# Kernel tuning notes

Hardware: AMD Instinct MI355X
Metric: run time of the kernel (lower is better)

Reference implementation:

```python
import jax, jax.numpy as jnp
import numpy as np

NEG_INF = -1e6  # d2l masked_softmax mask value

def setup_inputs() -> dict:
    key = jax.random.key(0)
    ks = jax.random.split(key, 6)
    B, Lq, Lk, dq, dv, H = 8, 256, 512, 256, 256, 64
    return {
        "queries": jax.random.normal(ks[0], (B, Lq, dq), jnp.float32),
        "keys": jax.random.normal(ks[1], (B, Lk, dq), jnp.float32),
        "values": jax.random.normal(ks[2], (B, Lk, dv), jnp.float32),
        "valid_lens": jax.random.randint(ks[3], (B,), 0, Lk),
        "W_q": jax.random.normal(ks[4], (H, dq), jnp.float32) * (dq ** -0.5),
        "W_k": jax.random.normal(ks[5], (H, dq), jnp.float32) * (dq ** -0.5),
        "w_v": jax.random.normal(jax.random.fold_in(key, 7), (H,), jnp.float32) * (H ** -0.5),
    }

def reference(queries, keys, values, valid_lens, W_q, W_k, w_v):
    # Project: [B,Lq,H], [B,Lk,H]
    q = jnp.einsum('bqd,hd->bqh', queries, W_q)
    k = jnp.einsum('bkd,hd->bkh', keys, W_k)
    # Broadcast-add + tanh: [B,Lq,Lk,H]
    features = jnp.tanh(q[:, :, None, :] + k[:, None, :, :])
    # Scalar projection -> scores [B,Lq,Lk]
    scores = jnp.einsum('bqkh,h->bqk', features, w_v)
    # masked_softmax over last axis with per-batch valid_lens
    Lk = keys.shape[1]
    mask = jnp.arange(Lk)[None, None, :] < valid_lens[:, None, None]
    scores = jnp.where(mask, scores, NEG_INF)
    attn = jax.nn.softmax(scores, axis=-1)
    # dropout p=0 (inference) -> identity; bmm with values
    return jnp.einsum('bqk,bkv->bqv', attn, values)
```

## Files before the change

### kernel.cpp

```cpp
#include <hip/hip_runtime.h>
#include <hip/hip_bf16.h>
#include <hip/hip_fp16.h>
#include <stdint.h>

#define NB 8
#define LQ 256
#define LK 512
#define NH 64
#define SCALE 2.8853900817779268f
#define L2E 1.4426950408889634f

#define QP_OFF   0
#define KP_OFF   131072
#define VBF_OFF  393216
#define PL_OFF   917504

extern "C" __device__ float __ocml_exp2_f32(float);
static __device__ __forceinline__ float fexp2(float x) {
#if __has_builtin(__builtin_amdgcn_exp2f)
  return __builtin_amdgcn_exp2f(x);
#else
  return __ocml_exp2_f32(x);
#endif
}
static __device__ __forceinline__ float frcp(float x) {
  return __builtin_amdgcn_rcpf(x);
}
static __device__ __forceinline__ uint16_t f2bf(float f) {
  uint32_t u = __float_as_uint(f);
  uint32_t r = (u + 0x7FFFu + ((u >> 16) & 1u)) >> 16;
  return (uint16_t)r;
}

typedef const __attribute__((address_space(1))) void* gas_ptr;
typedef __attribute__((address_space(3))) void* las_ptr;
static __device__ __forceinline__ void gload16(const void* g, void* l) {
  __builtin_amdgcn_global_load_lds((gas_ptr)g, (las_ptr)l, 16, 0, 0);
}

__global__ __launch_bounds__(256) void proj_kernel(
    const float* __restrict__ queries, const float* __restrict__ keys,
    const float* __restrict__ values,
    const float* __restrict__ Wq, const float* __restrict__ Wk,
    float* __restrict__ qp, float* __restrict__ kp, uint16_t* __restrict__ vbf)
{
  __shared__ float Wt[256][36];
  const int blk = blockIdx.x;
  const int t = threadIdx.x;

  if (blk >= 192) {
    int base = (blk - 192) * 16384 + t * 4;
#pragma unroll
    for (int it = 0; it < 16; ++it) {
      int idx = base + it * 1024;
      float4 v = *(const float4*)(values + idx);
      uint32_t lo = (uint32_t)f2bf(v.x) | ((uint32_t)f2bf(v.y) << 16);
      uint32_t hi = (uint32_t)f2bf(v.z) | ((uint32_t)f2bf(v.w) << 16);
      uint2 pk = {lo, hi};
      *(uint2*)(vbf + idx) = pk;
    }
    return;
  }

  const bool isQ = (blk < 64);
  const int sub = isQ ? blk : (blk - 64);
  const int tile = sub >> 1;
  const int hh = (sub & 1) * 32;
  const int rowbase = tile * 64;
  const float* __restrict__ X = isQ ? queries : keys;
  const float* __restrict__ W = isQ ? Wq : Wk;
  float* __restrict__ P = isQ ? qp : kp;

#pragma unroll 4
  for (int it = 0; it < 32; ++it) {
    Wt[t][it] = W[(hh + it) * 256 + t];
  }
  __syncthreads();

  const int ty = t >> 3;
  const int tx = t & 7;
  float a0x = 0.f, a0y = 0.f, a0z = 0.f, a0w = 0.f;
  float a1x = 0.f, a1y = 0.f, a1z = 0.f, a1w = 0.f;

  const float* xr0 = X + (size_t)(rowbase + ty * 2) * 256;
  const float* xr1 = xr0 + 256;

#pragma unroll 4
  for (int d4 = 0; d4 < 64; ++d4) {
    int d = d4 * 4;
    float4 x0 = *(const float4*)(xr0 + d);
    float4 x1 = *(const float4*)(xr1 + d);
    float4 w0 = *(const float4*)&Wt[d + 0][tx * 4];
    float4 w1 = *(const float4*)&Wt[d + 1][tx * 4];
    float4 w2 = *(const float4*)&Wt[d + 2][tx * 4];
    float4 w3 = *(const float4*)&Wt[d + 3][tx * 4];
#define STEP(XC, WD) \
    a0x = fmaf(x0.XC, WD.x, a0x); a0y = fmaf(x0.XC, WD.y, a0y); \
    a0z = fmaf(x0.XC, WD.z, a0z); a0w = fmaf(x0.XC, WD.w, a0w); \
    a1x = fmaf(x1.XC, WD.x, a1x); a1y = fmaf(x1.XC, WD.y, a1y); \
    a1z = fmaf(x1.XC, WD.z, a1z); a1w = fmaf(x1.XC, WD.w, a1w);
    STEP(x, w0) STEP(y, w1) STEP(z, w2) STEP(w, w3)
#undef STEP
  }

  {
    int row0 = rowbase + ty * 2;
    int h = hh + tx * 4;
    float4 o0 = {a0x * SCALE, a0y * SCALE, a0z * SCALE, a0w * SCALE};
    float4 o1 = {a1x * SCALE, a1y * SCALE, a1z * SCALE, a1w * SCALE};
    *(float4*)&P[(size_t)row0 * 64 + h] = o0;
    *(float4*)&P[(size_t)(row0 + 1) * 64 + h] = o1;
  }
}

__global__ __launch_bounds__(256) void attn_kernel(
    const float* __restrict__ qp, const float* __restrict__ kp,
    const uint16_t* __restrict__ vbf, const float* __restrict__ w_v,
    const int* __restrict__ valid_lens, float* __restrict__ out,
    float* __restrict__ pl, float* __restrict__ pacc, int nsplit)
{
  __shared__ float kTs[2][32][64];
  __shared__ uint16_t Vs[2][32][256];
  __shared__ float p_s[4][2][32];

  const int t = threadIdx.x;
  const int lane = t & 63;
  const int w = t >> 6;
  const int r2 = lane >> 5;
  const int kx = lane & 31;
  const int wg = blockIdx.x;
  const int b = wg & 7;
  const int qg = (wg >> 3) & 31;
  const int kh = wg >> 8;
  const int row = b * LQ + qg * 8 + w * 2 + r2;

  const int vl = valid_lens[b];
  const int n = (vl > 0) ? vl : LK;
  const int span = LK / nsplit;
  const int kstart = kh * span;
  int cnt = n - kstart;
  if (cnt > span) cnt = span;
  const int ntiles = (cnt > 0) ? ((cnt + 31) >> 5) : 0;

  if (ntiles == 0) {
    if (kx == 0) pl[row * nsplit + kh] = 0.f;
    float4 z = {0.f, 0.f, 0.f, 0.f};
    float* pa = pacc + ((size_t)(row * nsplit + kh)) * 256 + kx * 8;
    *(float4*)(pa + 0) = z;
    *(float4*)(pa + 4) = z;
    return;
  }

  float W1 = 0.f;
#pragma unroll
  for (int g = 0; g < 16; ++g) {
    float4 wf = *(const float4*)(w_v + g * 4);
    W1 += (wf.x + wf.y) + (wf.z + wf.w);
  }
  const float W1L = W1 * L2E;

  float qv[64];
  {
    const float* qrow = qp + (size_t)row * 64;
#pragma unroll
    for (int i = 0; i < 16; ++i) {
      float4 v = *(const float4*)(qrow + i * 4);
      qv[i * 4 + 0] = v.x; qv[i * 4 + 1] = v.y;
      qv[i * 4 + 2] = v.z; qv[i * 4 + 3] = v.w;
    }
  }

  const float* kpb = kp + (size_t)(b * LK) * 64;
  const char* vbc = (const char*)(vbf + (size_t)b * LK * 256);

#define STAGE(BUF, K0) do { \
    int i0 = w * 2; \
    int kjr0 = i0 * 4 + (lane >> 4); \
    int cph = lane & 15; \
    gload16(kpb + (size_t)((K0) + kjr0) * 64 + (cph ^ (kjr0 & 7)) * 4, \
            &kTs[BUF][i0 * 4][0]); \
    int kjr1 = kjr0 + 4; \
    gload16(kpb + (size_t)((K0) + kjr1) * 64 + (cph ^ (kjr1 & 7)) * 4, \
            &kTs[BUF][i0 * 4 + 4][0]); \
    const char* vsrc = vbc + (size_t)(K0) * 512 + (size_t)w * 4096 + lane * 16; \
    gload16(vsrc + 0 * 1024, &Vs[BUF][w * 8 + 0][0]); \
    gload16(vsrc + 1 * 1024, &Vs[BUF][w * 8 + 2][0]); \
    gload16(vsrc + 2 * 1024, &Vs[BUF][w * 8 + 4][0]); \
    gload16(vsrc + 3 * 1024, &Vs[BUF][w * 8 + 6][0]); \
  } while (0)

  float l = 0.f;
  float acc[16];
#pragma unroll
  for (int i = 0; i < 16; ++i) acc[i] = 0.f;

  STAGE(0, kstart);

  for (int tt = 0; tt < ntiles; ++tt) {
    const int cur = tt & 1;
    const int k0 = kstart + tt * 32;
    if (tt + 1 < ntiles) {
      STAGE(cur ^ 1, k0 + 32);
      asm volatile("s_waitcnt vmcnt(6)" ::: "memory");
    } else {
      asm volatile("s_waitcnt vmcnt(0)" ::: "memory");
    }
    __builtin_amdgcn_sched_barrier(0);
    __builtin_amdgcn_s_barrier();
    __builtin_amdgcn_sched_barrier(0);
    __builtin_amdgcn_s_setprio(1);

    float r0 = 0.f, r1 = 0.f, r2a = 0.f, r3 = 0.f;
#pragma unroll
    for (int g = 0; g < 16; ++g) {
      float4 kf = *(const float4*)&kTs[cur][kx][((g ^ (kx & 7)) << 2)];
      float4 wf = *(const float4*)(w_v + g * 4);
      r0  = fmaf(wf.x, frcp(1.f + fexp2(qv[g * 4 + 0] + kf.x)), r0);
      r1  = fmaf(wf.y, frcp(1.f + fexp2(qv[g * 4 + 1] + kf.y)), r1);
      r2a = fmaf(wf.z, frcp(1.f + fexp2(qv[g * 4 + 2] + kf.z)), r2a);
      r3  = fmaf(wf.w, frcp(1.f + fexp2(qv[g * 4 + 3] + kf.w)), r3);
    }
    float racc = (r0 + r1) + (r2a + r3);

    float pe = fexp2(fmaf(-SCALE, racc, W1L));
    int kg = k0 + kx;
    float p;
    if (vl == 0)      p = 1.f;
    else if (kg < n)  p = pe;
    else              p = 0.f;

    l += p;
    p_s[w][r2][kx] = p;

    const int c = kx;
#pragma unroll
    for (int i4 = 0; i4 < 4; ++i4) {
      float4 p0 = *(const float4*)&p_s[w][0][r2 * 16 + i4 * 4];
      float4 p1 = *(const float4*)&p_s[w][1][r2 * 16 + i4 * 4];
#pragma unroll
      for (int jj = 0; jj < 4; ++jj) {
        int kk = r2 * 16 + i4 * 4 + jj;
        uint4 vv = *(const uint4*)&Vs[cur][kk][c * 8];
        float pj0 = (jj == 0) ? p0.x : (jj == 1) ? p0.y : (jj == 2) ? p0.z : p0.w;
        float pj1 = (jj == 0) ? p1.x : (jj == 1) ? p1.y : (jj == 2) ? p1.z : p1.w;
        float f0 = __uint_as_float(vv.x << 16);
        float f1 = __uint_as_float(vv.x & 0xFFFF0000u);
        float f2 = __uint_as_float(vv.y << 16);
        float f3 = __uint_as_float(vv.y & 0xFFFF0000u);
        float f4 = __uint_as_float(vv.z << 16);
        float f5 = __uint_as_float(vv.z & 0xFFFF0000u);
        float f6 = __uint_as_float(vv.w << 16);
        float f7 = __uint_as_float(vv.w & 0xFFFF0000u);
        acc[0] = fmaf(pj0, f0, acc[0]);   acc[8]  = fmaf(pj1, f0, acc[8]);
        acc[1] = fmaf(pj0, f1, acc[1]);   acc[9]  = fmaf(pj1, f1, acc[9]);
        acc[2] = fmaf(pj0, f2, acc[2]);   acc[10] = fmaf(pj1, f2, acc[10]);
        acc[3] = fmaf(pj0, f3, acc[3]);   acc[11] = fmaf(pj1, f3, acc[11]);
        acc[4] = fmaf(pj0, f4, acc[4]);   acc[12] = fmaf(pj1, f4, acc[12]);
        acc[5] = fmaf(pj0, f5, acc[5]);   acc[13] = fmaf(pj1, f5, acc[13]);
        acc[6] = fmaf(pj0, f6, acc[6]);   acc[14] = fmaf(pj1, f6, acc[14]);
        acc[7] = fmaf(pj0, f7, acc[7]);   acc[15] = fmaf(pj1, f7, acc[15]);
      }
    }
    __builtin_amdgcn_s_setprio(0);
    __builtin_amdgcn_sched_barrier(0);
    __builtin_amdgcn_s_barrier();
  }
#undef STAGE

#pragma unroll
  for (int i = 0; i < 16; ++i) acc[i] += __shfl_xor(acc[i], 32, 64);
#pragma unroll
  for (int s = 16; s; s >>= 1) l += __shfl_xor(l, s, 64);

  const float* accr = acc + r2 * 8;
  if (nsplit == 1) {
    float inv = 1.f / l;
    float4 o0 = {accr[0] * inv, accr[1] * inv, accr[2] * inv, accr[3] * inv};
    float4 o1 = {accr[4] * inv, accr[5] * inv, accr[6] * inv, accr[7] * inv};
    float* op = out + (size_t)row * 256 + kx * 8;
    *(float4*)(op + 0) = o0;
    *(float4*)(op + 4) = o1;
  } else {
    if (kx == 0) pl[row * nsplit + kh] = l;
    float* pa = pacc + ((size_t)(row * nsplit + kh)) * 256 + kx * 8;
    float4 a0 = {accr[0], accr[1], accr[2], accr[3]};
    float4 a1 = {accr[4], accr[5], accr[6], accr[7]};
    *(float4*)(pa + 0) = a0;
    *(float4*)(pa + 4) = a1;
  }
}

__global__ __launch_bounds__(256) void merge_kernel(
    const float* __restrict__ pl, const float* __restrict__ pacc,
    float* __restrict__ out, int nsplit)
{
  const int t = threadIdx.x;
  const int row = blockIdx.x * 8 + (t >> 5);
  const int d8 = t & 31;

  float L = 0.f;
  float o[8];
#pragma unroll
  for (int i = 0; i < 8; ++i) o[i] = 0.f;

  for (int kh = 0; kh < nsplit; ++kh) {
    L += pl[row * nsplit + kh];
    const float* pa = pacc + ((size_t)(row * nsplit + kh)) * 256 + d8 * 8;
    float4 a0 = *(const float4*)(pa + 0);
    float4 a1 = *(const float4*)(pa + 4);
    o[0] += a0.x; o[1] += a0.y; o[2] += a0.z; o[3] += a0.w;
    o[4] += a1.x; o[5] += a1.y; o[6] += a1.z; o[7] += a1.w;
  }
  float inv = 1.f / L;
  float4 o0 = {o[0] * inv, o[1] * inv, o[2] * inv, o[3] * inv};
  float4 o1 = {o[4] * inv, o[5] * inv, o[6] * inv, o[7] * inv};
  float* op = out + (size_t)row * 256 + d8 * 8;
  *(float4*)(op + 0) = o0;
  *(float4*)(op + 4) = o1;
}

extern "C" void kernel_launch(void* const* d_in, const int* in_sizes, int n_in,
                              void* d_out, int out_size, void* d_ws, size_t ws_size,
                              hipStream_t stream) {
  const float* queries    = (const float*)d_in[0];
  const float* keys       = (const float*)d_in[1];
  const float* values     = (const float*)d_in[2];
  const int*   valid_lens = (const int*)d_in[3];
  const float* Wq         = (const float*)d_in[4];
  const float* Wk         = (const float*)d_in[5];
  const float* w_v        = (const float*)d_in[6];
  float* out = (float*)d_out;

  float* ws = (float*)d_ws;
  float* qp  = ws + QP_OFF;
  float* kp  = ws + KP_OFF;
  uint16_t* vbf = (uint16_t*)(ws + VBF_OFF);
  float* pl  = ws + PL_OFF;

  int nsplit;
  if      (ws_size >= (size_t)PL_OFF * 4 + 2048u * 4 * 4 + 2048u * 4 * 1024) nsplit = 4;
  else if (ws_size >= (size_t)PL_OFF * 4 + 2048u * 2 * 4 + 2048u * 2 * 1024) nsplit = 2;
  else nsplit = 1;
  float* pacc = pl + (size_t)2048 * nsplit;

  hipLaunchKernelGGL(proj_kernel, dim3(256), dim3(256), 0, stream,
                     queries, keys, values, Wq, Wk, qp, kp, vbf);
  hipLaunchKernelGGL(attn_kernel, dim3(nsplit * 256), dim3(256), 0, stream,
                     qp, kp, vbf, w_v, valid_lens, out, pl, pacc, nsplit);
  if (nsplit > 1) {
    hipLaunchKernelGGL(merge_kernel, dim3(256), dim3(256), 0, stream,
                       pl, pacc, out, nsplit);
  }
}
```

Baseline: 43.37 us.

## Use persistent attention blocks with an atomic work counter for load balancing

Replaces the one-block-per-unit grid with a fixed grid of 768 persistent blocks that pull (batch, query-group, key-split) work units from a global atomic counter reset by a memset before launch. The aim is to balance uneven per-unit work caused by variable valid_lens, and to let blocks that finish early on masked-out units pick up more work. It costs an extra memset launch, an atomic plus two block barriers per unit, and possibly worse register or scheduling behaviour from wrapping the kernel body in a loop.

New measurement: 44.92 us. +3.6%, slower.

```diff
diff --git a/kernel.cpp b/kernel.cpp
--- a/kernel.cpp
+++ b/kernel.cpp
@@ -13,7 +13,7 @@
 #define QP_OFF   0
 #define KP_OFF   131072
 #define VBF_OFF  393216
-#define PL_OFF   917504
+#define CTR_OFF  917504
 
 extern "C" __device__ float __ocml_exp2_f32(float);
 static __device__ __forceinline__ float fexp2(float x) {
@@ -117,39 +117,21 @@
     const float* __restrict__ qp, const float* __restrict__ kp,
     const uint16_t* __restrict__ vbf, const float* __restrict__ w_v,
     const int* __restrict__ valid_lens, float* __restrict__ out,
-    float* __restrict__ pl, float* __restrict__ pacc, int nsplit)
+    uint32_t* __restrict__ ctr, float* __restrict__ pl,
+    float* __restrict__ pacc, int nsplit)
 {
   __shared__ float kTs[2][32][64];
   __shared__ uint16_t Vs[2][32][256];
   __shared__ float p_s[4][2][32];
+  __shared__ uint32_t unit_s;
 
   const int t = threadIdx.x;
   const int lane = t & 63;
   const int w = t >> 6;
   const int r2 = lane >> 5;
   const int kx = lane & 31;
-  const int wg = blockIdx.x;
-  const int b = wg & 7;
-  const int qg = (wg >> 3) & 31;
-  const int kh = wg >> 8;
-  const int row = b * LQ + qg * 8 + w * 2 + r2;
-
-  const int vl = valid_lens[b];
-  const int n = (vl > 0) ? vl : LK;
+  const uint32_t NU = 256u * (uint32_t)nsplit;
   const int span = LK / nsplit;
-  const int kstart = kh * span;
-  int cnt = n - kstart;
-  if (cnt > span) cnt = span;
-  const int ntiles = (cnt > 0) ? ((cnt + 31) >> 5) : 0;
-
-  if (ntiles == 0) {
-    if (kx == 0) pl[row * nsplit + kh] = 0.f;
-    float4 z = {0.f, 0.f, 0.f, 0.f};
-    float* pa = pacc + ((size_t)(row * nsplit + kh)) * 256 + kx * 8;
-    *(float4*)(pa + 0) = z;
-    *(float4*)(pa + 4) = z;
-    return;
-  }
 
   float W1 = 0.f;
 #pragma unroll
@@ -159,19 +141,47 @@
   }
   const float W1L = W1 * L2E;
 
-  float qv[64];
-  {
-    const float* qrow = qp + (size_t)row * 64;
-#pragma unroll
-    for (int i = 0; i < 16; ++i) {
-      float4 v = *(const float4*)(qrow + i * 4);
-      qv[i * 4 + 0] = v.x; qv[i * 4 + 1] = v.y;
-      qv[i * 4 + 2] = v.z; qv[i * 4 + 3] = v.w;
-    }
-  }
-
-  const float* kpb = kp + (size_t)(b * LK) * 64;
-  const char* vbc = (const char*)(vbf + (size_t)b * LK * 256);
+  for (;;) {
+    if (t == 0) unit_s = atomicAdd(ctr, 1u);
+    __syncthreads();
+    const uint32_t u = unit_s;
+    __syncthreads();
+    if (u >= NU) break;
+
+    const int b = u & 7;
+    const int qg = (u >> 3) & 31;
+    const int kh = u >> 8;
+    const int row = b * LQ + qg * 8 + w * 2 + r2;
+
+    const int vl = valid_lens[b];
+    const int n = (vl > 0) ? vl : LK;
+    const int kstart = kh * span;
+    int cnt = n - kstart;
+    if (cnt > span) cnt = span;
+    const int ntiles = (cnt > 0) ? ((cnt + 31) >> 5) : 0;
+
+    if (ntiles == 0) {
+      if (kx == 0) pl[row * nsplit + kh] = 0.f;
+      float4 z = {0.f, 0.f, 0.f, 0.f};
+      float* pa = pacc + ((size_t)(row * nsplit + kh)) * 256 + kx * 8;
+      *(float4*)(pa + 0) = z;
+      *(float4*)(pa + 4) = z;
+      continue;
+    }
+
+    float qv[64];
+    {
+      const float* qrow = qp + (size_t)row * 64;
+#pragma unroll
+      for (int i = 0; i < 16; ++i) {
+        float4 v = *(const float4*)(qrow + i * 4);
+        qv[i * 4 + 0] = v.x; qv[i * 4 + 1] = v.y;
+        qv[i * 4 + 2] = v.z; qv[i * 4 + 3] = v.w;
+      }
+    }
+
+    const float* kpb = kp + (size_t)(b * LK) * 64;
+    const char* vbc = (const char*)(vbf + (size_t)b * LK * 256);
 
 #define STAGE(BUF, K0) do { \
     int i0 = w * 2; \
@@ -189,104 +199,105 @@
     gload16(vsrc + 3 * 1024, &Vs[BUF][w * 8 + 6][0]); \
   } while (0)
 
-  float l = 0.f;
-  float acc[16];
-#pragma unroll
-  for (int i = 0; i < 16; ++i) acc[i] = 0.f;
-
-  STAGE(0, kstart);
-
-  for (int tt = 0; tt < ntiles; ++tt) {
-    const int cur = tt & 1;
-    const int k0 = kstart + tt * 32;
-    if (tt + 1 < ntiles) {
-      STAGE(cur ^ 1, k0 + 32);
-      asm volatile("s_waitcnt vmcnt(6)" ::: "memory");
+    float l = 0.f;
+    float acc[16];
+#pragma unroll
+    for (int i = 0; i < 16; ++i) acc[i] = 0.f;
+
+    STAGE(0, kstart);
+
+    for (int tt = 0; tt < ntiles; ++tt) {
+      const int cur = tt & 1;
+      const int k0 = kstart + tt * 32;
+      if (tt + 1 < ntiles) {
+        STAGE(cur ^ 1, k0 + 32);
+        asm volatile("s_waitcnt vmcnt(6)" ::: "memory");
+      } else {
+        asm volatile("s_waitcnt vmcnt(0)" ::: "memory");
+      }
+      __builtin_amdgcn_sched_barrier(0);
+      __builtin_amdgcn_s_barrier();
+      __builtin_amdgcn_sched_barrier(0);
+      __builtin_amdgcn_s_setprio(1);
+
+      float r0 = 0.f, r1 = 0.f, r2a = 0.f, r3 = 0.f;
+#pragma unroll
+      for (int g = 0; g < 16; ++g) {
+        float4 kf = *(const float4*)&kTs[cur][kx][((g ^ (kx & 7)) << 2)];
+        float4 wf = *(const float4*)(w_v + g * 4);
+        r0  = fmaf(wf.x, frcp(1.f + fexp2(qv[g * 4 + 0] + kf.x)), r0);
+        r1  = fmaf(wf.y, frcp(1.f + fexp2(qv[g * 4 + 1] + kf.y)), r1);
+        r2a = fmaf(wf.z, frcp(1.f + fexp2(qv[g * 4 + 2] + kf.z)), r2a);
+        r3  = fmaf(wf.w, frcp(1.f + fexp2(qv[g * 4 + 3] + kf.w)), r3);
+      }
+      float racc = (r0 + r1) + (r2a + r3);
+
+      float pe = fexp2(fmaf(-SCALE, racc, W1L));
+      int kg = k0 + kx;
+      float p;
+      if (vl == 0)      p = 1.f;
+      else if (kg < n)  p = pe;
+      else              p = 0.f;
+
+      l += p;
+      p_s[w][r2][kx] = p;
+
+      const int c = kx;
+#pragma unroll
+      for (int i4 = 0; i4 < 4; ++i4) {
+        float4 p0 = *(const float4*)&p_s[w][0][r2 * 16 + i4 * 4];
+        float4 p1 = *(const float4*)&p_s[w][1][r2 * 16 + i4 * 4];
+#pragma unroll
+        for (int jj = 0; jj < 4; ++jj) {
+          int kk = r2 * 16 + i4 * 4 + jj;
+          uint4 vv = *(const uint4*)&Vs[cur][kk][c * 8];
+          float pj0 = (jj == 0) ? p0.x : (jj == 1) ? p0.y : (jj == 2) ? p0.z : p0.w;
+          float pj1 = (jj == 0) ? p1.x : (jj == 1) ? p1.y : (jj == 2) ? p1.z : p1.w;
+          float f0 = __uint_as_float(vv.x << 16);
+          float f1 = __uint_as_float(vv.x & 0xFFFF0000u);
+          float f2 = __uint_as_float(vv.y << 16);
+          float f3 = __uint_as_float(vv.y & 0xFFFF0000u);
+          float f4 = __uint_as_float(vv.z << 16);
+          float f5 = __uint_as_float(vv.z & 0xFFFF0000u);
+          float f6 = __uint_as_float(vv.w << 16);
+          float f7 = __uint_as_float(vv.w & 0xFFFF0000u);
+          acc[0] = fmaf(pj0, f0, acc[0]);   acc[8]  = fmaf(pj1, f0, acc[8]);
+          acc[1] = fmaf(pj0, f1, acc[1]);   acc[9]  = fmaf(pj1, f1, acc[9]);
+          acc[2] = fmaf(pj0, f2, acc[2]);   acc[10] = fmaf(pj1, f2, acc[10]);
+          acc[3] = fmaf(pj0, f3, acc[3]);   acc[11] = fmaf(pj1, f3, acc[11]);
+          acc[4] = fmaf(pj0, f4, acc[4]);   acc[12] = fmaf(pj1, f4, acc[12]);
+          acc[5] = fmaf(pj0, f5, acc[5]);   acc[13] = fmaf(pj1, f5, acc[13]);
+          acc[6] = fmaf(pj0, f6, acc[6]);   acc[14] = fmaf(pj1, f6, acc[14]);
+          acc[7] = fmaf(pj0, f7, acc[7]);   acc[15] = fmaf(pj1, f7, acc[15]);
+        }
+      }
+      __builtin_amdgcn_s_setprio(0);
+      __builtin_amdgcn_sched_barrier(0);
+      __builtin_amdgcn_s_barrier();
+    }
+#undef STAGE
+
+#pragma unroll
+    for (int i = 0; i < 16; ++i) acc[i] += __shfl_xor(acc[i], 32, 64);
+#pragma unroll
+    for (int s = 16; s; s >>= 1) l += __shfl_xor(l, s, 64);
+
+    const float* accr = acc + r2 * 8;
+    if (nsplit == 1) {
+      float inv = 1.f / l;
+      float4 o0 = {accr[0] * inv, accr[1] * inv, accr[2] * inv, accr[3] * inv};
+      float4 o1 = {accr[4] * inv, accr[5] * inv, accr[6] * inv, accr[7] * inv};
+      float* op = out + (size_t)row * 256 + kx * 8;
+      *(float4*)(op + 0) = o0;
+      *(float4*)(op + 4) = o1;
     } else {
-      asm volatile("s_waitcnt vmcnt(0)" ::: "memory");
-    }
-    __builtin_amdgcn_sched_barrier(0);
-    __builtin_amdgcn_s_barrier();
-    __builtin_amdgcn_sched_barrier(0);
-    __builtin_amdgcn_s_setprio(1);
-
-    float r0 = 0.f, r1 = 0.f, r2a = 0.f, r3 = 0.f;
-#pragma unroll
-    for (int g = 0; g < 16; ++g) {
-      float4 kf = *(const float4*)&kTs[cur][kx][((g ^ (kx & 7)) << 2)];
-      float4 wf = *(const float4*)(w_v + g * 4);
-      r0  = fmaf(wf.x, frcp(1.f + fexp2(qv[g * 4 + 0] + kf.x)), r0);
-      r1  = fmaf(wf.y, frcp(1.f + fexp2(qv[g * 4 + 1] + kf.y)), r1);
-      r2a = fmaf(wf.z, frcp(1.f + fexp2(qv[g * 4 + 2] + kf.z)), r2a);
-      r3  = fmaf(wf.w, frcp(1.f + fexp2(qv[g * 4 + 3] + kf.w)), r3);
-    }
-    float racc = (r0 + r1) + (r2a + r3);
-
-    float pe = fexp2(fmaf(-SCALE, racc, W1L));
-    int kg = k0 + kx;
-    float p;
-    if (vl == 0)      p = 1.f;
-    else if (kg < n)  p = pe;
-    else              p = 0.f;
-
-    l += p;
-    p_s[w][r2][kx] = p;
-
-    const int c = kx;
-#pragma unroll
-    for (int i4 = 0; i4 < 4; ++i4) {
-      float4 p0 = *(const float4*)&p_s[w][0][r2 * 16 + i4 * 4];
-      float4 p1 = *(const float4*)&p_s[w][1][r2 * 16 + i4 * 4];
-#pragma unroll
-      for (int jj = 0; jj < 4; ++jj) {
-        int kk = r2 * 16 + i4 * 4 + jj;
-        uint4 vv = *(const uint4*)&Vs[cur][kk][c * 8];
-        float pj0 = (jj == 0) ? p0.x : (jj == 1) ? p0.y : (jj == 2) ? p0.z : p0.w;
-        float pj1 = (jj == 0) ? p1.x : (jj == 1) ? p1.y : (jj == 2) ? p1.z : p1.w;
-        float f0 = __uint_as_float(vv.x << 16);
-        float f1 = __uint_as_float(vv.x & 0xFFFF0000u);
-        float f2 = __uint_as_float(vv.y << 16);
-        float f3 = __uint_as_float(vv.y & 0xFFFF0000u);
-        float f4 = __uint_as_float(vv.z << 16);
-        float f5 = __uint_as_float(vv.z & 0xFFFF0000u);
-        float f6 = __uint_as_float(vv.w << 16);
-        float f7 = __uint_as_float(vv.w & 0xFFFF0000u);
-        acc[0] = fmaf(pj0, f0, acc[0]);   acc[8]  = fmaf(pj1, f0, acc[8]);
-        acc[1] = fmaf(pj0, f1, acc[1]);   acc[9]  = fmaf(pj1, f1, acc[9]);
-        acc[2] = fmaf(pj0, f2, acc[2]);   acc[10] = fmaf(pj1, f2, acc[10]);
-        acc[3] = fmaf(pj0, f3, acc[3]);   acc[11] = fmaf(pj1, f3, acc[11]);
-        acc[4] = fmaf(pj0, f4, acc[4]);   acc[12] = fmaf(pj1, f4, acc[12]);
-        acc[5] = fmaf(pj0, f5, acc[5]);   acc[13] = fmaf(pj1, f5, acc[13]);
-        acc[6] = fmaf(pj0, f6, acc[6]);   acc[14] = fmaf(pj1, f6, acc[14]);
-        acc[7] = fmaf(pj0, f7, acc[7]);   acc[15] = fmaf(pj1, f7, acc[15]);
-      }
-    }
-    __builtin_amdgcn_s_setprio(0);
-    __builtin_amdgcn_sched_barrier(0);
-    __builtin_amdgcn_s_barrier();
-  }
-#undef STAGE
-
-#pragma unroll
-  for (int i = 0; i < 16; ++i) acc[i] += __shfl_xor(acc[i], 32, 64);
-#pragma unroll
-  for (int s = 16; s; s >>= 1) l += __shfl_xor(l, s, 64);
-
-  const float* accr = acc + r2 * 8;
-  if (nsplit == 1) {
-    float inv = 1.f / l;
-    float4 o0 = {accr[0] * inv, accr[1] * inv, accr[2] * inv, accr[3] * inv};
-    float4 o1 = {accr[4] * inv, accr[5] * inv, accr[6] * inv, accr[7] * inv};
-    float* op = out + (size_t)row * 256 + kx * 8;
-    *(float4*)(op + 0) = o0;
-    *(float4*)(op + 4) = o1;
-  } else {
-    if (kx == 0) pl[row * nsplit + kh] = l;
-    float* pa = pacc + ((size_t)(row * nsplit + kh)) * 256 + kx * 8;
-    float4 a0 = {accr[0], accr[1], accr[2], accr[3]};
-    float4 a1 = {accr[4], accr[5], accr[6], accr[7]};
-    *(float4*)(pa + 0) = a0;
-    *(float4*)(pa + 4) = a1;
+      if (kx == 0) pl[row * nsplit + kh] = l;
+      float* pa = pacc + ((size_t)(row * nsplit + kh)) * 256 + kx * 8;
+      float4 a0 = {accr[0], accr[1], accr[2], accr[3]};
+      float4 a1 = {accr[4], accr[5], accr[6], accr[7]};
+      *(float4*)(pa + 0) = a0;
+      *(float4*)(pa + 4) = a1;
+    }
   }
 }
 
@@ -335,18 +346,20 @@
   float* qp  = ws + QP_OFF;
   float* kp  = ws + KP_OFF;
   uint16_t* vbf = (uint16_t*)(ws + VBF_OFF);
-  float* pl  = ws + PL_OFF;
+  uint32_t* ctr = (uint32_t*)(ws + CTR_OFF);
 
   int nsplit;
-  if      (ws_size >= (size_t)PL_OFF * 4 + 2048u * 4 * 4 + 2048u * 4 * 1024) nsplit = 4;
-  else if (ws_size >= (size_t)PL_OFF * 4 + 2048u * 2 * 4 + 2048u * 2 * 1024) nsplit = 2;
+  if      (ws_size >= (size_t)CTR_OFF * 4 + 64 + 2048u * 4 * 4 + 2048u * 4 * 1024) nsplit = 4;
+  else if (ws_size >= (size_t)CTR_OFF * 4 + 64 + 2048u * 2 * 4 + 2048u * 2 * 1024) nsplit = 2;
   else nsplit = 1;
+  float* pl   = ws + CTR_OFF + 16;
   float* pacc = pl + (size_t)2048 * nsplit;
 
   hipLaunchKernelGGL(proj_kernel, dim3(256), dim3(256), 0, stream,
                      queries, keys, values, Wq, Wk, qp, kp, vbf);
-  hipLaunchKernelGGL(attn_kernel, dim3(nsplit * 256), dim3(256), 0, stream,
-                     qp, kp, vbf, w_v, valid_lens, out, pl, pacc, nsplit);
+  hipMemsetAsync(ctr, 0, 4, stream);
+  hipLaunchKernelGGL(attn_kernel, dim3(768), dim3(256), 0, stream,
+                     qp, kp, vbf, w_v, valid_lens, out, ctr, pl, pacc, nsplit);
   if (nsplit > 1) {
     hipLaunchKernelGGL(merge_kernel, dim3(256), dim3(256), 0, stream,
                        pl, pacc, out, nsplit);
```

## Fuse split-K merge into attention kernel via last-block atomic counter

Applied to the files above, without the earlier changes.

Removes the separate merge kernel launch. Each attention workgroup writes its partial sums, fences, and atomically increments a per-(batch, query-group) counter. The last arriving split does the reduction and normalisation. Empty splits now skip writing zero partial accumulators, and the merge skips partials whose l is zero. The counters are reset in proj_kernel, at the cost of a threadfence and atomic per block and a serialized tail merge.

Result: slower. 165.1 us (+280.7%).

```diff
diff --git a/kernel.cpp b/kernel.cpp
--- a/kernel.cpp
+++ b/kernel.cpp
@@ -42,11 +42,14 @@
     const float* __restrict__ queries, const float* __restrict__ keys,
     const float* __restrict__ values,
     const float* __restrict__ Wq, const float* __restrict__ Wk,
-    float* __restrict__ qp, float* __restrict__ kp, uint16_t* __restrict__ vbf)
+    float* __restrict__ qp, float* __restrict__ kp, uint16_t* __restrict__ vbf,
+    uint32_t* __restrict__ cnt)
 {
   __shared__ float Wt[256][36];
   const int blk = blockIdx.x;
   const int t = threadIdx.x;
+
+  if (t == 0) cnt[blk] = 0;
 
   if (blk >= 192) {
     int base = (blk - 192) * 16384 + t * 4;
@@ -117,11 +120,13 @@
     const float* __restrict__ qp, const float* __restrict__ kp,
     const uint16_t* __restrict__ vbf, const float* __restrict__ w_v,
     const int* __restrict__ valid_lens, float* __restrict__ out,
-    float* __restrict__ pl, float* __restrict__ pacc, int nsplit)
+    float* __restrict__ pl, float* __restrict__ pacc,
+    uint32_t* __restrict__ cnt, int nsplit)
 {
   __shared__ float kTs[2][32][64];
   __shared__ uint16_t Vs[2][32][256];
   __shared__ float p_s[4][2][32];
+  __shared__ uint32_t old_s;
 
   const int t = threadIdx.x;
   const int lane = t & 63;
@@ -138,40 +143,37 @@
   const int n = (vl > 0) ? vl : LK;
   const int span = LK / nsplit;
   const int kstart = kh * span;
-  int cnt = n - kstart;
-  if (cnt > span) cnt = span;
-  const int ntiles = (cnt > 0) ? ((cnt + 31) >> 5) : 0;
-
-  if (ntiles == 0) {
-    if (kx == 0) pl[row * nsplit + kh] = 0.f;
-    float4 z = {0.f, 0.f, 0.f, 0.f};
-    float* pa = pacc + ((size_t)(row * nsplit + kh)) * 256 + kx * 8;
-    *(float4*)(pa + 0) = z;
-    *(float4*)(pa + 4) = z;
-    return;
-  }
-
-  float W1 = 0.f;
-#pragma unroll
-  for (int g = 0; g < 16; ++g) {
-    float4 wf = *(const float4*)(w_v + g * 4);
-    W1 += (wf.x + wf.y) + (wf.z + wf.w);
-  }
-  const float W1L = W1 * L2E;
-
-  float qv[64];
-  {
-    const float* qrow = qp + (size_t)row * 64;
-#pragma unroll
-    for (int i = 0; i < 16; ++i) {
-      float4 v = *(const float4*)(qrow + i * 4);
-      qv[i * 4 + 0] = v.x; qv[i * 4 + 1] = v.y;
-      qv[i * 4 + 2] = v.z; qv[i * 4 + 3] = v.w;
-    }
-  }
-
-  const float* kpb = kp + (size_t)(b * LK) * 64;
-  const char* vbc = (const char*)(vbf + (size_t)b * LK * 256);
+  int cnt_k = n - kstart;
+  if (cnt_k > span) cnt_k = span;
+  const int ntiles = (cnt_k > 0) ? ((cnt_k + 31) >> 5) : 0;
+
+  float l = 0.f;
+  float acc[16];
+#pragma unroll
+  for (int i = 0; i < 16; ++i) acc[i] = 0.f;
+
+  if (ntiles > 0) {
+    float W1 = 0.f;
+#pragma unroll
+    for (int g = 0; g < 16; ++g) {
+      float4 wf = *(const float4*)(w_v + g * 4);
+      W1 += (wf.x + wf.y) + (wf.z + wf.w);
+    }
+    const float W1L = W1 * L2E;
+
+    float qv[64];
+    {
+      const float* qrow = qp + (size_t)row * 64;
+#pragma unroll
+      for (int i = 0; i < 16; ++i) {
+        float4 v = *(const float4*)(qrow + i * 4);
+        qv[i * 4 + 0] = v.x; qv[i * 4 + 1] = v.y;
+        qv[i * 4 + 2] = v.z; qv[i * 4 + 3] = v.w;
+      }
+    }
+
+    const float* kpb = kp + (size_t)(b * LK) * 64;
+    const char* vbc = (const char*)(vbf + (size_t)b * LK * 256);
 
 #define STAGE(BUF, K0) do { \
     int i0 = w * 2; \
@@ -189,88 +191,84 @@
     gload16(vsrc + 3 * 1024, &Vs[BUF][w * 8 + 6][0]); \
   } while (0)
 
-  float l = 0.f;
-  float acc[16];
-#pragma unroll
-  for (int i = 0; i < 16; ++i) acc[i] = 0.f;
-
-  STAGE(0, kstart);
-
-  for (int tt = 0; tt < ntiles; ++tt) {
-    const int cur = tt & 1;
-    const int k0 = kstart + tt * 32;
-    if (tt + 1 < ntiles) {
-      STAGE(cur ^ 1, k0 + 32);
-      asm volatile("s_waitcnt vmcnt(6)" ::: "memory");
-    } else {
-      asm volatile("s_waitcnt vmcnt(0)" ::: "memory");
-    }
-    __builtin_amdgcn_sched_barrier(0);
-    __builtin_amdgcn_s_barrier();
-    __builtin_amdgcn_sched_barrier(0);
-    __builtin_amdgcn_s_setprio(1);
-
-    float r0 = 0.f, r1 = 0.f, r2a = 0.f, r3 = 0.f;
-#pragma unroll
-    for (int g = 0; g < 16; ++g) {
-      float4 kf = *(const float4*)&kTs[cur][kx][((g ^ (kx & 7)) << 2)];
-      float4 wf = *(const float4*)(w_v + g * 4);
-      r0  = fmaf(wf.x, frcp(1.f + fexp2(qv[g * 4 + 0] + kf.x)), r0);
-      r1  = fmaf(wf.y, frcp(1.f + fexp2(qv[g * 4 + 1] + kf.y)), r1);
-      r2a = fmaf(wf.z, frcp(1.f + fexp2(qv[g * 4 + 2] + kf.z)), r2a);
-      r3  = fmaf(wf.w, frcp(1.f + fexp2(qv[g * 4 + 3] + kf.w)), r3);
-    }
-    float racc = (r0 + r1) + (r2a + r3);
-
-    float pe = fexp2(fmaf(-SCALE, racc, W1L));
-    int kg = k0 + kx;
-    float p;
-    if (vl == 0)      p = 1.f;
-    else if (kg < n)  p = pe;
-    else              p = 0.f;
-
-    l += p;
-    p_s[w][r2][kx] = p;
-
-    const int c = kx;
-#pragma unroll
-    for (int i4 = 0; i4 < 4; ++i4) {
-      float4 p0 = *(const float4*)&p_s[w][0][r2 * 16 + i4 * 4];
-      float4 p1 = *(const float4*)&p_s[w][1][r2 * 16 + i4 * 4];
-#pragma unroll
-      for (int jj = 0; jj < 4; ++jj) {
-        int kk = r2 * 16 + i4 * 4 + jj;
-        uint4 vv = *(const uint4*)&Vs[cur][kk][c * 8];
-        float pj0 = (jj == 0) ? p0.x : (jj == 1) ? p0.y : (jj == 2) ? p0.z : p0.w;
-        float pj1 = (jj == 0) ? p1.x : (jj == 1) ? p1.y : (jj == 2) ? p1.z : p1.w;
-        float f0 = __uint_as_float(vv.x << 16);
-        float f1 = __uint_as_float(vv.x & 0xFFFF0000u);
-        float f2 = __uint_as_float(vv.y << 16);
-        float f3 = __uint_as_float(vv.y & 0xFFFF0000u);
-        float f4 = __uint_as_float(vv.z << 16);
-        float f5 = __uint_as_float(vv.z & 0xFFFF0000u);
-        float f6 = __uint_as_float(vv.w << 16);
-        float f7 = __uint_as_float(vv.w & 0xFFFF0000u);
-        acc[0] = fmaf(pj0, f0, acc[0]);   acc[8]  = fmaf(pj1, f0, acc[8]);
-        acc[1] = fmaf(pj0, f1, acc[1]);   acc[9]  = fmaf(pj1, f1, acc[9]);
-        acc[2] = fmaf(pj0, f2, acc[2]);   acc[10] = fmaf(pj1, f2, acc[10]);
-        acc[3] = fmaf(pj0, f3, acc[3]);   acc[11] = fmaf(pj1, f3, acc[11]);
-        acc[4] = fmaf(pj0, f4, acc[4]);   acc[12] = fmaf(pj1, f4, acc[12]);
-        acc[5] = fmaf(pj0, f5, acc[5]);   acc[13] = fmaf(pj1, f5, acc[13]);
-        acc[6] = fmaf(pj0, f6, acc[6]);   acc[14] = fmaf(pj1, f6, acc[14]);
-        acc[7] = fmaf(pj0, f7, acc[7]);   acc[15] = fmaf(pj1, f7, acc[15]);
-      }
-    }
-    __builtin_amdgcn_s_setprio(0);
-    __builtin_amdgcn_sched_barrier(0);
-    __builtin_amdgcn_s_barrier();
-  }
+    STAGE(0, kstart);
+
+    for (int tt = 0; tt < ntiles; ++tt) {
+      const int cur = tt & 1;
+      const int k0 = kstart + tt * 32;
+      if (tt + 1 < ntiles) {
+        STAGE(cur ^ 1, k0 + 32);
+        asm volatile("s_waitcnt vmcnt(6)" ::: "memory");
+      } else {
+        asm volatile("s_waitcnt vmcnt(0)" ::: "memory");
+      }
+      __builtin_amdgcn_sched_barrier(0);
+      __builtin_amdgcn_s_barrier();
+      __builtin_amdgcn_sched_barrier(0);
+      __builtin_amdgcn_s_setprio(1);
+
+      float r0 = 0.f, r1 = 0.f, r2a = 0.f, r3 = 0.f;
+#pragma unroll
+      for (int g = 0; g < 16; ++g) {
+        float4 kf = *(const float4*)&kTs[cur][kx][((g ^ (kx & 7)) << 2)];
+        float4 wf = *(const float4*)(w_v + g * 4);
+        r0  = fmaf(wf.x, frcp(1.f + fexp2(qv[g * 4 + 0] + kf.x)), r0);
+        r1  = fmaf(wf.y, frcp(1.f + fexp2(qv[g * 4 + 1] + kf.y)), r1);
+        r2a = fmaf(wf.z, frcp(1.f + fexp2(qv[g * 4 + 2] + kf.z)), r2a);
+        r3  = fmaf(wf.w, frcp(1.f + fexp2(qv[g * 4 + 3] + kf.w)), r3);
+      }
+      float racc = (r0 + r1) + (r2a + r3);
+
+      float pe = fexp2(fmaf(-SCALE, racc, W1L));
+      int kg = k0 + kx;
+      float p;
+      if (vl == 0)      p = 1.f;
+      else if (kg < n)  p = pe;
+      else              p = 0.f;
+
+      l += p;
+      p_s[w][r2][kx] = p;
+
+      const int c = kx;
+#pragma unroll
+      for (int i4 = 0; i4 < 4; ++i4) {
+        float4 p0 = *(const float4*)&p_s[w][0][r2 * 16 + i4 * 4];
+        float4 p1 = *(const float4*)&p_s[w][1][r2 * 16 + i4 * 4];
+#pragma unroll
+        for (int jj = 0; jj < 4; ++jj) {
+          int kk = r2 * 16 + i4 * 4 + jj;
+          uint4 vv = *(const uint4*)&Vs[cur][kk][c * 8];
+          float pj0 = (jj == 0) ? p0.x : (jj == 1) ? p0.y : (jj == 2) ? p0.z : p0.w;
+          float pj1 = (jj == 0) ? p1.x : (jj == 1) ? p1.y : (jj == 2) ? p1.z : p1.w;
+          float f0 = __uint_as_float(vv.x << 16);
+          float f1 = __uint_as_float(vv.x & 0xFFFF0000u);
+          float f2 = __uint_as_float(vv.y << 16);
+          float f3 = __uint_as_float(vv.y & 0xFFFF0000u);
+          float f4 = __uint_as_float(vv.z << 16);
+          float f5 = __uint_as_float(vv.z & 0xFFFF0000u);
+          float f6 = __uint_as_float(vv.w << 16);
+          float f7 = __uint_as_float(vv.w & 0xFFFF0000u);
+          acc[0] = fmaf(pj0, f0, acc[0]);   acc[8]  = fmaf(pj1, f0, acc[8]);
+          acc[1] = fmaf(pj0, f1, acc[1]);   acc[9]  = fmaf(pj1, f1, acc[9]);
+          acc[2] = fmaf(pj0, f2, acc[2]);   acc[10] = fmaf(pj1, f2, acc[10]);
+          acc[3] = fmaf(pj0, f3, acc[3]);   acc[11] = fmaf(pj1, f3, acc[11]);
+          acc[4] = fmaf(pj0, f4, acc[4]);   acc[12] = fmaf(pj1, f4, acc[12]);
+          acc[5] = fmaf(pj0, f5, acc[5]);   acc[13] = fmaf(pj1, f5, acc[13]);
+          acc[6] = fmaf(pj0, f6, acc[6]);   acc[14] = fmaf(pj1, f6, acc[14]);
+          acc[7] = fmaf(pj0, f7, acc[7]);   acc[15] = fmaf(pj1, f7, acc[15]);
+        }
+      }
+      __builtin_amdgcn_s_setprio(0);
+      __builtin_amdgcn_sched_barrier(0);
+      __builtin_amdgcn_s_barrier();
+    }
 #undef STAGE
 
 #pragma unroll
-  for (int i = 0; i < 16; ++i) acc[i] += __shfl_xor(acc[i], 32, 64);
-#pragma unroll
-  for (int s = 16; s; s >>= 1) l += __shfl_xor(l, s, 64);
+    for (int i = 0; i < 16; ++i) acc[i] += __shfl_xor(acc[i], 32, 64);
+#pragma unroll
+    for (int s = 16; s; s >>= 1) l += __shfl_xor(l, s, 64);
+  }
 
   const float* accr = acc + r2 * 8;
   if (nsplit == 1) {
@@ -280,43 +278,50 @@
     float* op = out + (size_t)row * 256 + kx * 8;
     *(float4*)(op + 0) = o0;
     *(float4*)(op + 4) = o1;
-  } else {
-    if (kx == 0) pl[row * nsplit + kh] = l;
+    return;
+  }
+
+  if (kx == 0) pl[row * nsplit + kh] = l;
+  if (ntiles > 0) {
     float* pa = pacc + ((size_t)(row * nsplit + kh)) * 256 + kx * 8;
     float4 a0 = {accr[0], accr[1], accr[2], accr[3]};
     float4 a1 = {accr[4], accr[5], accr[6], accr[7]};
     *(float4*)(pa + 0) = a0;
     *(float4*)(pa + 4) = a1;
   }
-}
-
-__global__ __launch_bounds__(256) void merge_kernel(
-    const float* __restrict__ pl, const float* __restrict__ pacc,
-    float* __restrict__ out, int nsplit)
-{
-  const int t = threadIdx.x;
-  const int row = blockIdx.x * 8 + (t >> 5);
-  const int d8 = t & 31;
-
-  float L = 0.f;
-  float o[8];
-#pragma unroll
-  for (int i = 0; i < 8; ++i) o[i] = 0.f;
-
-  for (int kh = 0; kh < nsplit; ++kh) {
-    L += pl[row * nsplit + kh];
-    const float* pa = pacc + ((size_t)(row * nsplit + kh)) * 256 + d8 * 8;
-    float4 a0 = *(const float4*)(pa + 0);
-    float4 a1 = *(const float4*)(pa + 4);
-    o[0] += a0.x; o[1] += a0.y; o[2] += a0.z; o[3] += a0.w;
-    o[4] += a1.x; o[5] += a1.y; o[6] += a1.z; o[7] += a1.w;
-  }
-  float inv = 1.f / L;
-  float4 o0 = {o[0] * inv, o[1] * inv, o[2] * inv, o[3] * inv};
-  float4 o1 = {o[4] * inv, o[5] * inv, o[6] * inv, o[7] * inv};
-  float* op = out + (size_t)row * 256 + d8 * 8;
-  *(float4*)(op + 0) = o0;
-  *(float4*)(op + 4) = o1;
+
+  __threadfence();
+  __syncthreads();
+  if (t == 0) old_s = atomicAdd(&cnt[(b << 5) | qg], 1u);
+  __syncthreads();
+  if (old_s != (uint32_t)(nsplit - 1)) return;
+
+  __threadfence();
+  {
+    const int mrow = b * LQ + qg * 8 + (t >> 5);
+    const int d8 = t & 31;
+    float L = 0.f;
+    float o[8];
+#pragma unroll
+    for (int i = 0; i < 8; ++i) o[i] = 0.f;
+    for (int kh2 = 0; kh2 < nsplit; ++kh2) {
+      float lk = pl[mrow * nsplit + kh2];
+      if (lk > 0.f) {
+        L += lk;
+        const float* pa = pacc + ((size_t)(mrow * nsplit + kh2)) * 256 + d8 * 8;
+        float4 a0 = *(const float4*)(pa + 0);
+        float4 a1 = *(const float4*)(pa + 4);
+        o[0] += a0.x; o[1] += a0.y; o[2] += a0.z; o[3] += a0.w;
+        o[4] += a1.x; o[5] += a1.y; o[6] += a1.z; o[7] += a1.w;
+      }
+    }
+    float inv = 1.f / L;
+    float4 o0 = {o[0] * inv, o[1] * inv, o[2] * inv, o[3] * inv};
+    float4 o1 = {o[4] * inv, o[5] * inv, o[6] * inv, o[7] * inv};
+    float* op = out + (size_t)mrow * 256 + d8 * 8;
+    *(float4*)(op + 0) = o0;
+    *(float4*)(op + 4) = o1;
+  }
 }
 
 extern "C" void kernel_launch(void* const* d_in, const int* in_sizes, int n_in,
@@ -338,17 +343,14 @@
   float* pl  = ws + PL_OFF;
 
   int nsplit;
-  if      (ws_size >= (size_t)PL_OFF * 4 + 2048u * 4 * 4 + 2048u * 4 * 1024) nsplit = 4;
-  else if (ws_size >= (size_t)PL_OFF * 4 + 2048u * 2 * 4 + 2048u * 2 * 1024) nsplit = 2;
+  if      (ws_size >= (size_t)PL_OFF * 4 + 2048u * 4 * 4 + 2048u * 4 * 1024 + 1024) nsplit = 4;
+  else if (ws_size >= (size_t)PL_OFF * 4 + 2048u * 2 * 4 + 2048u * 2 * 1024 + 1024) nsplit = 2;
   else nsplit = 1;
   float* pacc = pl + (size_t)2048 * nsplit;
+  uint32_t* cnt = (uint32_t*)(pacc + (size_t)2048 * nsplit * 256);
 
   hipLaunchKernelGGL(proj_kernel, dim3(256), dim3(256), 0, stream,
-                     queries, keys, values, Wq, Wk, qp, kp, vbf);
+                     queries, keys, values, Wq, Wk, qp, kp, vbf, cnt);
   hipLaunchKernelGGL(attn_kernel, dim3(nsplit * 256), dim3(256), 0, stream,
-                     qp, kp, vbf, w_v, valid_lens, out, pl, pacc, nsplit);
-  if (nsplit > 1) {
-    hipLaunchKernelGGL(merge_kernel, dim3(256), dim3(256), 0, stream,
-                       pl, pacc, out, nsplit);
-  }
-}
+                     qp, kp, vbf, w_v, valid_lens, out, pl, pacc, cnt, nsplit);
+}
```

## Single-buffer K/V shared tiles and issue first stage before Q load

Applied to the files above, without the earlier changes.

Replaces the double-buffered K/V shared-memory staging with a single buffer. The next tile's loads are now issued only after the end-of-iteration barrier, and the loop waits for all loads before computing. The first stage is moved ahead of the W1 and Q register loads so it overlaps them. This halves LDS use, which may raise occupancy, but it gives up overlapping the next tile's global loads with the current tile's compute.

Measured after the change: 44.34 us. 2.2% more time.

```diff
diff --git a/kernel.cpp b/kernel.cpp
--- a/kernel.cpp
+++ b/kernel.cpp
@@ -119,8 +119,8 @@
     const int* __restrict__ valid_lens, float* __restrict__ out,
     float* __restrict__ pl, float* __restrict__ pacc, int nsplit)
 {
-  __shared__ float kTs[2][32][64];
-  __shared__ uint16_t Vs[2][32][256];
+  __shared__ float kTs[32][64];
+  __shared__ uint16_t Vs[32][256];
   __shared__ float p_s[4][2][32];
 
   const int t = threadIdx.x;
@@ -151,6 +151,27 @@
     return;
   }
 
+  const float* kpb = kp + (size_t)(b * LK) * 64;
+  const char* vbc = (const char*)(vbf + (size_t)b * LK * 256);
+
+#define STAGE(K0) do { \
+    int i0 = w * 2; \
+    int kjr0 = i0 * 4 + (lane >> 4); \
+    int cph = lane & 15; \
+    gload16(kpb + (size_t)((K0) + kjr0) * 64 + (cph ^ (kjr0 & 7)) * 4, \
+            &kTs[i0 * 4][0]); \
+    int kjr1 = kjr0 + 4; \
+    gload16(kpb + (size_t)((K0) + kjr1) * 64 + (cph ^ (kjr1 & 7)) * 4, \
+            &kTs[i0 * 4 + 4][0]); \
+    const char* vsrc = vbc + (size_t)(K0) * 512 + (size_t)w * 4096 + lane * 16; \
+    gload16(vsrc + 0 * 1024, &Vs[w * 8 + 0][0]); \
+    gload16(vsrc + 1 * 1024, &Vs[w * 8 + 2][0]); \
+    gload16(vsrc + 2 * 1024, &Vs[w * 8 + 4][0]); \
+    gload16(vsrc + 3 * 1024, &Vs[w * 8 + 6][0]); \
+  } while (0)
+
+  STAGE(kstart);
+
   float W1 = 0.f;
 #pragma unroll
   for (int g = 0; g < 16; ++g) {
@@ -170,41 +191,14 @@
     }
   }
 
-  const float* kpb = kp + (size_t)(b * LK) * 64;
-  const char* vbc = (const char*)(vbf + (size_t)b * LK * 256);
-
-#define STAGE(BUF, K0) do { \
-    int i0 = w * 2; \
-    int kjr0 = i0 * 4 + (lane >> 4); \
-    int cph = lane & 15; \
-    gload16(kpb + (size_t)((K0) + kjr0) * 64 + (cph ^ (kjr0 & 7)) * 4, \
-            &kTs[BUF][i0 * 4][0]); \
-    int kjr1 = kjr0 + 4; \
-    gload16(kpb + (size_t)((K0) + kjr1) * 64 + (cph ^ (kjr1 & 7)) * 4, \
-            &kTs[BUF][i0 * 4 + 4][0]); \
-    const char* vsrc = vbc + (size_t)(K0) * 512 + (size_t)w * 4096 + lane * 16; \
-    gload16(vsrc + 0 * 1024, &Vs[BUF][w * 8 + 0][0]); \
-    gload16(vsrc + 1 * 1024, &Vs[BUF][w * 8 + 2][0]); \
-    gload16(vsrc + 2 * 1024, &Vs[BUF][w * 8 + 4][0]); \
-    gload16(vsrc + 3 * 1024, &Vs[BUF][w * 8 + 6][0]); \
-  } while (0)
-
   float l = 0.f;
   float acc[16];
 #pragma unroll
   for (int i = 0; i < 16; ++i) acc[i] = 0.f;
 
-  STAGE(0, kstart);
-
   for (int tt = 0; tt < ntiles; ++tt) {
-    const int cur = tt & 1;
     const int k0 = kstart + tt * 32;
-    if (tt + 1 < ntiles) {
-      STAGE(cur ^ 1, k0 + 32);
-      asm volatile("s_waitcnt vmcnt(6)" ::: "memory");
-    } else {
-      asm volatile("s_waitcnt vmcnt(0)" ::: "memory");
-    }
+    asm volatile("s_waitcnt vmcnt(0)" ::: "memory");
     __builtin_amdgcn_sched_barrier(0);
     __builtin_amdgcn_s_barrier();
     __builtin_amdgcn_sched_barrier(0);
@@ -213,7 +207,7 @@
     float r0 = 0.f, r1 = 0.f, r2a = 0.f, r3 = 0.f;
 #pragma unroll
     for (int g = 0; g < 16; ++g) {
-      float4 kf = *(const float4*)&kTs[cur][kx][((g ^ (kx & 7)) << 2)];
+      float4 kf = *(const float4*)&kTs[kx][((g ^ (kx & 7)) << 2)];
       float4 wf = *(const float4*)(w_v + g * 4);
       r0  = fmaf(wf.x, frcp(1.f + fexp2(qv[g * 4 + 0] + kf.x)), r0);
       r1  = fmaf(wf.y, frcp(1.f + fexp2(qv[g * 4 + 1] + kf.y)), r1);
@@ -240,7 +234,7 @@
 #pragma unroll
       for (int jj = 0; jj < 4; ++jj) {
         int kk = r2 * 16 + i4 * 4 + jj;
-        uint4 vv = *(const uint4*)&Vs[cur][kk][c * 8];
+        uint4 vv = *(const uint4*)&Vs[kk][c * 8];
         float pj0 = (jj == 0) ? p0.x : (jj == 1) ? p0.y : (jj == 2) ? p0.z : p0.w;
         float pj1 = (jj == 0) ? p1.x : (jj == 1) ? p1.y : (jj == 2) ? p1.z : p1.w;
         float f0 = __uint_as_float(vv.x << 16);
@@ -264,6 +258,7 @@
     __builtin_amdgcn_s_setprio(0);
     __builtin_amdgcn_sched_barrier(0);
     __builtin_amdgcn_s_barrier();
+    if (tt + 1 < ntiles) STAGE(k0 + 32);
   }
 #undef STAGE
 
```
